# Kernel optimization log

Hardware: AMD Instinct MI355X
Metric: run time of the kernel (lower is better)

Reference implementation:

```python
import jax, jax.numpy as jnp
import numpy as np

N_NODES = 50000
N_EDGES = 400000
HEADS = 3
CH = 128
NEG_SLOPE = 0.2
EPS = 1e-16


def setup_inputs() -> dict:
    key = jax.random.key(0)
    ks = jax.random.split(key, 10)
    return {
        "x": jax.random.normal(ks[0], (N_NODES, 9), jnp.float32),
        "emb_w": jax.random.normal(ks[1], (9, 128), jnp.float32) * 0.1,
        "emb_b": jax.random.normal(ks[2], (128,), jnp.float32) * 0.1,
        "gat_w": jax.random.normal(ks[3], (128, HEADS * CH), jnp.float32) * 0.05,
        "att_src": jax.random.normal(ks[4], (HEADS, CH), jnp.float32) * 0.1,
        "att_dst": jax.random.normal(ks[5], (HEADS, CH), jnp.float32) * 0.1,
        "gat_bias": jax.random.normal(ks[6], (CH,), jnp.float32) * 0.1,
        "out_w": jax.random.normal(ks[7], (128, 4), jnp.float32) * 0.1,
        "out_b": jax.random.normal(ks[8], (4,), jnp.float32) * 0.1,
        "edge_index": jax.random.randint(ks[9], (2, N_EDGES), 0, N_NODES, jnp.int64 if jax.config.jax_enable_x64 else jnp.int32),
    }


def reference(x, emb_w, emb_b, gat_w, att_src, att_dst, gat_bias, out_w, out_b, edge_index):
    n = x.shape[0]
    h = x @ emb_w + emb_b                                   # [N,128]
    # add self loops (PyG GATConv default)
    loops = jnp.arange(n, dtype=edge_index.dtype)
    src = jnp.concatenate([edge_index[0], loops])
    dst = jnp.concatenate([edge_index[1], loops])
    xh = (h @ gat_w).reshape(n, HEADS, CH)                  # [N,H,C]
    a_src = jnp.einsum('nhc,hc->nh', xh, att_src)           # [N,H]
    a_dst = jnp.einsum('nhc,hc->nh', xh, att_dst)           # [N,H]
    e = a_src[src] + a_dst[dst]                             # [E,H]
    e = jax.nn.leaky_relu(e, NEG_SLOPE)
    # segment softmax over destination node
    e_max = jax.ops.segment_max(e, dst, num_segments=n)
    e = jnp.exp(e - e_max[dst])
    denom = jax.ops.segment_sum(e, dst, num_segments=n)
    alpha = e / (denom[dst] + EPS)                          # [E,H]
    msg = xh[src] * alpha[:, :, None]                       # [E,H,C]
    agg = jax.ops.segment_sum(msg, dst, num_segments=n)     # [N,H,C]
    out = agg.mean(axis=1) + gat_bias                       # concat=False -> head mean
    x_new = out + h                                         # residual
    return x_new @ out_w + out_b                            # [N,4]
```

## Files before the change

kernel.cpp:

```cpp
#include <hip/hip_runtime.h>
#include <hip/hip_bf16.h>
#include <cstdint>

#define NB 8
#define NEG 0.2f
#define SBS 256
#define SCAN2_T 1024
#define PADK 56

typedef __attribute__((ext_vector_type(8))) short bf16x8;
typedef __attribute__((ext_vector_type(4))) float f32x4;

__device__ __forceinline__ float bf2f(unsigned short u){
  return __uint_as_float(((unsigned)u)<<16);
}
__device__ __forceinline__ unsigned short f2bf(float f){
  __hip_bfloat16 b = __float2bfloat16(f);
  return *reinterpret_cast<unsigned short*>(&b);
}

__global__ __launch_bounds__(256)
void watt_kernel(const float* __restrict__ gat_w, const float* __restrict__ att_src,
                 const float* __restrict__ att_dst, float* __restrict__ w_att_s,
                 float* __restrict__ w_att_d)
{
  int wave = threadIdx.x >> 6, lane = threadIdx.x & 63;
  int o = blockIdx.x*4 + wave;
  if (o >= 768) return;
  int isD = (o >= 384);
  int t = isD ? (o - 384) : o;
  int h = t >> 7, k = t & 127;
  const float* att = isD ? att_dst : att_src;
  int c = 2*lane;
  float g0 = gat_w[(size_t)k*384 + h*128 + c];
  float g1 = gat_w[(size_t)k*384 + h*128 + c + 1];
  float dot = g0*att[h*128+c] + g1*att[h*128+c+1];
  #pragma unroll
  for (int off=32; off; off>>=1) dot += __shfl_down(dot, off);
  if (lane==0){
    if (isD) w_att_d[t] = dot; else w_att_s[t] = dot;
  }
}

__global__ __launch_bounds__(256)
void bt_kernel(const float* __restrict__ gat_w, unsigned short* __restrict__ Bt2)
{
  int i = blockIdx.x*256 + threadIdx.x;
  if (i >= 12*128*32) return;
  int ks  = i >> 12;
  int rem = i & 4095;
  int col = rem >> 5;
  int kk  = rem & 31;
  int t = ks*32 + kk;
  int h = t >> 7, k = t & 127;
  Bt2[i] = f2bf(gat_w[(size_t)k*384 + h*128 + col] * (1.f/3.f));
}

__global__ __launch_bounds__(128)
void embed_kernel(const float* __restrict__ x, const float* __restrict__ emb_w,
                  const float* __restrict__ emb_b, const float* __restrict__ w_att_s,
                  const float* __restrict__ w_att_d,
                  unsigned short* __restrict__ h_bf, float* __restrict__ a_s,
                  float* __restrict__ a_d, int nN)
{
  __shared__ float xs[NB][12];
  int t = threadIdx.x;
  int n0 = blockIdx.x * NB;

  if (t < NB*9){
    int j = t/9, k = t - j*9;
    int n = n0 + j;
    xs[j][k] = (n < nN) ? x[(size_t)n*9 + k] : 0.f;
  }
  __syncthreads();

  float bb = emb_b[t];
  float ws0=w_att_s[t], ws1=w_att_s[128+t], ws2=w_att_s[256+t];
  float wd0=w_att_d[t], wd1=w_att_d[128+t], wd2=w_att_d[256+t];

  float hv[NB];
  #pragma unroll
  for (int j=0;j<NB;j++){
    float acc = bb;
    #pragma unroll
    for (int k=0;k<9;k++) acc += xs[j][k]*emb_w[k*128+t];
    hv[j] = acc;
    int n = n0 + j;
    if (n < nN) h_bf[(size_t)n*128 + t] = f2bf(acc);
  }

  __shared__ float red[2][NB][6];
  int wv = t>>6, ln = t&63;
  #pragma unroll
  for (int j=0;j<NB;j++){
    float pr[6] = {hv[j]*ws0, hv[j]*ws1, hv[j]*ws2,
                   hv[j]*wd0, hv[j]*wd1, hv[j]*wd2};
    #pragma unroll
    for (int off=32; off; off>>=1){
      #pragma unroll
      for (int i=0;i<6;i++) pr[i] += __shfl_down(pr[i], off);
    }
    if (ln==0){
      #pragma unroll
      for (int i=0;i<6;i++) red[wv][j][i]=pr[i];
    }
  }
  __syncthreads();
  if (t < NB*6){
    int j=t/6, i=t-j*6;
    int n=n0+j;
    if (n<nN){
      float v = red[0][j][i]+red[1][j][i];
      if (i<3) a_s[(size_t)n*3+i]=v; else a_d[(size_t)n*3+(i-3)]=v;
    }
  }
}

__global__ __launch_bounds__(256)
void deg_kernel(const int* __restrict__ ei, int* __restrict__ deg, int nE)
{
  int e = blockIdx.x*256 + threadIdx.x;
  if (e < nE) atomicAdd(&deg[ei[nE + e]], 1);
}

__global__ __launch_bounds__(SBS)
void blocksum_kernel(const int* __restrict__ deg, int* __restrict__ bsum, int nN)
{
  int i = blockIdx.x*SBS + threadIdx.x;
  int v = (i < nN) ? deg[i] : 0;
  #pragma unroll
  for (int off=32; off; off>>=1) v += __shfl_down(v, off);
  __shared__ int ws[SBS/64];
  if ((threadIdx.x&63)==0) ws[threadIdx.x>>6] = v;
  __syncthreads();
  if (threadIdx.x==0){
    int s=0;
    #pragma unroll
    for (int i2=0;i2<SBS/64;i2++) s += ws[i2];
    bsum[blockIdx.x]=s;
  }
}

__global__ __launch_bounds__(SCAN2_T)
void scansum_kernel(const int* __restrict__ bsum, int* __restrict__ boff, int nB)
{
  __shared__ int s[SCAN2_T];
  int t = threadIdx.x;
  int v = (t < nB) ? bsum[t] : 0;
  s[t] = v;
  __syncthreads();
  for (int off=1; off<SCAN2_T; off<<=1){
    int add = (t >= off) ? s[t-off] : 0;
    __syncthreads();
    s[t] += add;
    __syncthreads();
  }
  if (t < nB) boff[t] = (t==0) ? 0 : s[t-1];
}

__global__ __launch_bounds__(SBS)
void blockscan_kernel(const int* __restrict__ deg, const int* __restrict__ boff,
                      int* __restrict__ rowptr, int* __restrict__ cursor, int nN)
{
  __shared__ int s[SBS];
  int t = threadIdx.x;
  int i = blockIdx.x*SBS + t;
  int v = (i < nN) ? deg[i] : 0;
  s[t] = v;
  __syncthreads();
  for (int off=1; off<SBS; off<<=1){
    int add = (t >= off) ? s[t-off] : 0;
    __syncthreads();
    s[t] += add;
    __syncthreads();
  }
  int excl = boff[blockIdx.x] + ((t==0) ? 0 : s[t-1]);
  if (i < nN){ rowptr[i] = excl; cursor[i] = excl; }
  if (i == nN-1) rowptr[nN] = excl + v;
}

__global__ __launch_bounds__(256)
void scatter_kernel(const int* __restrict__ ei, int* __restrict__ cursor,
                    int* __restrict__ csr, int nE)
{
  int e = blockIdx.x*256 + threadIdx.x;
  if (e < nE){
    int s = ei[e], d = ei[nE + e];
    int pos = atomicAdd(&cursor[d], 1);
    csr[pos] = s;
  }
}

__global__ __launch_bounds__(256)
void gather_kernel(const int* __restrict__ rowptr, const int* __restrict__ csr,
                   const float* __restrict__ a_s, const float* __restrict__ a_d,
                   const unsigned short* __restrict__ h_bf,
                   unsigned short* __restrict__ hagg, int nN)
{
  int wave = threadIdx.x >> 6, lane = threadIdx.x & 63;
  int n = blockIdx.x*4 + wave;
  if (n >= nN) return;

  int ro  = rowptr[n];
  int deg = rowptr[n+1] - ro;
  int degT = deg + 1;
  float ad0 = a_d[(size_t)n*3+0], ad1 = a_d[(size_t)n*3+1], ad2 = a_d[(size_t)n*3+2];

  float d0=0.f, d1=0.f, d2=0.f;
  float acc00=0.f, acc01=0.f, acc10=0.f, acc11=0.f, acc20=0.f, acc21=0.f;

  for (int base=0; base<degT; base+=64){
    int i = base + lane;
    int sReg = n; float p0=0.f, p1=0.f, p2=0.f;
    if (i < degT){
      int s = (i < deg) ? csr[ro+i] : n;
      sReg = s;
      float e0 = a_s[(size_t)s*3+0] + ad0; e0 = e0>0.f ? e0 : NEG*e0;
      float e1 = a_s[(size_t)s*3+1] + ad1; e1 = e1>0.f ? e1 : NEG*e1;
      float e2 = a_s[(size_t)s*3+2] + ad2; e2 = e2>0.f ? e2 : NEG*e2;
      p0 = __expf(e0); p1 = __expf(e1); p2 = __expf(e2);
      d0 += p0; d1 += p1; d2 += p2;
    }
    int cnt = min(64, degT - base);
    for (int j=0;j<cnt;j++){
      int   s  = __shfl(sReg, j);
      float A0 = __shfl(p0, j);
      float A1 = __shfl(p1, j);
      float A2 = __shfl(p2, j);
      ushort2 hv = *(const ushort2*)(h_bf + (size_t)s*128 + 2*lane);
      float f0 = bf2f(hv.x), f1 = bf2f(hv.y);
      acc00 += A0*f0; acc01 += A0*f1;
      acc10 += A1*f0; acc11 += A1*f1;
      acc20 += A2*f0; acc21 += A2*f1;
    }
  }
  #pragma unroll
  for (int off=1; off<64; off<<=1){
    d0 += __shfl_xor(d0, off);
    d1 += __shfl_xor(d1, off);
    d2 += __shfl_xor(d2, off);
  }
  float w0 = 1.f/(d0+1e-16f);
  float w1 = 1.f/(d1+1e-16f);
  float w2 = 1.f/(d2+1e-16f);

  size_t base = (size_t)n*384 + 2*lane;
  ushort2 o0 = {f2bf(acc00*w0), f2bf(acc01*w0)};
  ushort2 o1 = {f2bf(acc10*w1), f2bf(acc11*w1)};
  ushort2 o2 = {f2bf(acc20*w2), f2bf(acc21*w2)};
  *(ushort2*)(hagg + base      ) = o0;
  *(ushort2*)(hagg + base + 128) = o1;
  *(ushort2*)(hagg + base + 256) = o2;
}

__global__ __launch_bounds__(256)
void gemm2_kernel(const unsigned short* __restrict__ hagg,
                  const unsigned short* __restrict__ Bt2,
                  const unsigned short* __restrict__ h_bf,
                  const float* __restrict__ gat_bias,
                  const float* __restrict__ out_w, const float* __restrict__ out_b,
                  float* __restrict__ out, int nN)
{
  __shared__ __align__(16) unsigned short Bs[2][128*PADK];
  int tid  = threadIdx.x;
  int wave = tid >> 6, lane = tid & 63;
  int cl = lane & 15, kg = lane >> 4;
  int r0 = blockIdx.x*64 + wave*16;
  int rowA = min(r0 + cl, nN-1);
  const unsigned short* aBase = hagg + (size_t)rowA*384 + kg*8;

  int scol = tid >> 1, shalf = tid & 1;
  int dstI = scol*(PADK/8) + shalf*2;

  {
    const int4* src = (const int4*)Bt2;
    int4 t0 = src[2*tid], t1 = src[2*tid+1];
    ((int4*)Bs[0])[dstI]   = t0;
    ((int4*)Bs[0])[dstI+1] = t1;
  }
  f32x4 acc[8];
  #pragma unroll
  for (int f=0;f<8;f++) acc[f] = (f32x4){0.f,0.f,0.f,0.f};
  bf16x8 aCur = *(const bf16x8*)(aBase);
  __syncthreads();

  #pragma unroll
  for (int ks=0; ks<12; ks++){
    int4 t0, t1; bf16x8 aNext;
    if (ks < 11){
      const int4* src = (const int4*)(Bt2 + (size_t)(ks+1)*4096);
      t0 = src[2*tid]; t1 = src[2*tid+1];
      aNext = *(const bf16x8*)(aBase + (ks+1)*32);
    }
    const unsigned short* bs = Bs[ks & 1];
    #pragma unroll
    for (int f=0;f<8;f++){
      bf16x8 b = *(const bf16x8*)(bs + (f*16 + cl)*PADK + kg*8);
      acc[f] = __builtin_amdgcn_mfma_f32_16x16x32_bf16(aCur, b, acc[f], 0, 0, 0);
    }
    if (ks < 11){
      int4* dst = (int4*)Bs[(ks+1) & 1];
      dst[dstI]   = t0;
      dst[dstI+1] = t1;
      aCur = aNext;
    }
    __syncthreads();
  }

  float p[4][4];
  #pragma unroll
  for (int r=0;r<4;r++)
    #pragma unroll
    for (int j=0;j<4;j++) p[r][j]=0.f;

  #pragma unroll
  for (int f=0;f<8;f++){
    int col = f*16 + cl;
    float bias = gat_bias[col];
    float w0=out_w[col*4+0], w1=out_w[col*4+1], w2=out_w[col*4+2], w3=out_w[col*4+3];
    #pragma unroll
    for (int r=0;r<4;r++){
      int row = r0 + kg*4 + r;
      float hres = (row < nN) ? bf2f(h_bf[(size_t)row*128 + col]) : 0.f;
      float xn = acc[f][r] + bias + hres;
      p[r][0] += xn*w0; p[r][1] += xn*w1; p[r][2] += xn*w2; p[r][3] += xn*w3;
    }
  }
  #pragma unroll
  for (int off=1; off<16; off<<=1){
    #pragma unroll
    for (int r=0;r<4;r++)
      #pragma unroll
      for (int j=0;j<4;j++) p[r][j] += __shfl_xor(p[r][j], off);
  }
  if (cl == 0){
    #pragma unroll
    for (int r=0;r<4;r++){
      int row = r0 + kg*4 + r;
      if (row < nN){
        float4 o = {p[r][0]+out_b[0], p[r][1]+out_b[1], p[r][2]+out_b[2], p[r][3]+out_b[3]};
        *(float4*)(out + (size_t)row*4) = o;
      }
    }
  }
}

extern "C" void kernel_launch(void* const* d_in, const int* in_sizes, int n_in,
                              void* d_out, int out_size, void* d_ws, size_t ws_size,
                              hipStream_t stream) {
  const float* x       = (const float*)d_in[0];
  const float* emb_w   = (const float*)d_in[1];
  const float* emb_b   = (const float*)d_in[2];
  const float* gat_w   = (const float*)d_in[3];
  const float* att_src = (const float*)d_in[4];
  const float* att_dst = (const float*)d_in[5];
  const float* gat_bias= (const float*)d_in[6];
  const float* out_w   = (const float*)d_in[7];
  const float* out_b   = (const float*)d_in[8];
  const int*   ei      = (const int*)d_in[9];
  float* out = (float*)d_out;

  int nN = in_sizes[0]/9;
  int nE = in_sizes[9]/2;
  int nB = (nN + SBS - 1) / SBS;

  char* p = (char*)d_ws;
  auto alloc = [&](size_t bytes)->char*{
    char* r = p; p += (bytes + 255) & ~(size_t)255; return r;
  };
  unsigned short* h_bf   = (unsigned short*)alloc((size_t)nN*128*2);
  float*          a_s    = (float*)         alloc((size_t)nN*3*4);
  float*          a_d    = (float*)         alloc((size_t)nN*3*4);
  float*          w_att_s= (float*)         alloc(384*4);
  float*          w_att_d= (float*)         alloc(384*4);
  unsigned short* Bt2    = (unsigned short*)alloc((size_t)12*128*32*2);
  int*            deg    = (int*)           alloc((size_t)nN*4);
  int*            rowptr = (int*)           alloc(((size_t)nN+1)*4);
  int*            cursor = (int*)           alloc((size_t)nN*4);
  int*            csr    = (int*)           alloc((size_t)nE*4);
  int*            bsum   = (int*)           alloc((size_t)nB*4);
  int*            boff   = (int*)           alloc((size_t)nB*4);
  unsigned short* hagg   = (unsigned short*)alloc((size_t)nN*384*2);

  hipMemsetAsync(deg, 0, (size_t)nN*4, stream);

  watt_kernel<<<192, 256, 0, stream>>>(gat_w, att_src, att_dst, w_att_s, w_att_d);
  bt_kernel<<<(12*128*32+255)/256, 256, 0, stream>>>(gat_w, Bt2);

  embed_kernel<<<(nN+NB-1)/NB, 128, 0, stream>>>(
      x, emb_w, emb_b, w_att_s, w_att_d, h_bf, a_s, a_d, nN);

  deg_kernel<<<(nE+255)/256, 256, 0, stream>>>(ei, deg, nE);
  blocksum_kernel<<<nB, SBS, 0, stream>>>(deg, bsum, nN);
  scansum_kernel<<<1, SCAN2_T, 0, stream>>>(bsum, boff, nB);
  blockscan_kernel<<<nB, SBS, 0, stream>>>(deg, boff, rowptr, cursor, nN);
  scatter_kernel<<<(nE+255)/256, 256, 0, stream>>>(ei, cursor, csr, nE);

  gather_kernel<<<(nN+3)/4, 256, 0, stream>>>(
      rowptr, csr, a_s, a_d, h_bf, hagg, nN);

  gemm2_kernel<<<(nN+63)/64, 256, 0, stream>>>(
      hagg, Bt2, h_bf, gat_bias, out_w, out_b, out, nN);
}
```

Baseline: 245.8 us.

## Merge weight-prep kernels and compute embedding one node per thread

Fuses the attention-weight and B-transpose preparation kernels into a single launch that branches on block index. Rewrites the embedding kernel so each thread handles a whole node: it computes all 128 channels serially, packs bf16 outputs into 16-byte stores, and accumulates the six attention dot products in registers. This drops the shared-memory staging, the cross-lane shuffles and the block barriers. The trade-off is far fewer threads (about 196 blocks) with serial per-thread work and strided per-node row writes, which may underuse the GPU and coalesce poorly.

```diff
diff --git a/kernel.cpp b/kernel.cpp
--- a/kernel.cpp
+++ b/kernel.cpp
@@ -2,7 +2,6 @@
 #include <hip/hip_bf16.h>
 #include <cstdint>
 
-#define NB 8
 #define NEG 0.2f
 #define SBS 256
 #define SCAN2_T 1024
@@ -20,100 +19,74 @@
 }
 
 __global__ __launch_bounds__(256)
-void watt_kernel(const float* __restrict__ gat_w, const float* __restrict__ att_src,
+void prep_kernel(const float* __restrict__ gat_w, const float* __restrict__ att_src,
                  const float* __restrict__ att_dst, float* __restrict__ w_att_s,
-                 float* __restrict__ w_att_d)
-{
-  int wave = threadIdx.x >> 6, lane = threadIdx.x & 63;
-  int o = blockIdx.x*4 + wave;
-  if (o >= 768) return;
-  int isD = (o >= 384);
-  int t = isD ? (o - 384) : o;
-  int h = t >> 7, k = t & 127;
-  const float* att = isD ? att_dst : att_src;
-  int c = 2*lane;
-  float g0 = gat_w[(size_t)k*384 + h*128 + c];
-  float g1 = gat_w[(size_t)k*384 + h*128 + c + 1];
-  float dot = g0*att[h*128+c] + g1*att[h*128+c+1];
-  #pragma unroll
-  for (int off=32; off; off>>=1) dot += __shfl_down(dot, off);
-  if (lane==0){
-    if (isD) w_att_d[t] = dot; else w_att_s[t] = dot;
-  }
-}
-
-__global__ __launch_bounds__(256)
-void bt_kernel(const float* __restrict__ gat_w, unsigned short* __restrict__ Bt2)
-{
-  int i = blockIdx.x*256 + threadIdx.x;
-  if (i >= 12*128*32) return;
-  int ks  = i >> 12;
-  int rem = i & 4095;
-  int col = rem >> 5;
-  int kk  = rem & 31;
-  int t = ks*32 + kk;
-  int h = t >> 7, k = t & 127;
-  Bt2[i] = f2bf(gat_w[(size_t)k*384 + h*128 + col] * (1.f/3.f));
-}
-
-__global__ __launch_bounds__(128)
+                 float* __restrict__ w_att_d, unsigned short* __restrict__ Bt2)
+{
+  if (blockIdx.x < 192){
+    int wave = threadIdx.x >> 6, lane = threadIdx.x & 63;
+    int o = blockIdx.x*4 + wave;
+    if (o >= 768) return;
+    int isD = (o >= 384);
+    int t = isD ? (o - 384) : o;
+    int h = t >> 7, k = t & 127;
+    const float* att = isD ? att_dst : att_src;
+    int c = 2*lane;
+    float g0 = gat_w[(size_t)k*384 + h*128 + c];
+    float g1 = gat_w[(size_t)k*384 + h*128 + c + 1];
+    float dot = g0*att[h*128+c] + g1*att[h*128+c+1];
+    #pragma unroll
+    for (int off=32; off; off>>=1) dot += __shfl_down(dot, off);
+    if (lane==0){
+      if (isD) w_att_d[t] = dot; else w_att_s[t] = dot;
+    }
+  } else {
+    int i = (blockIdx.x-192)*256 + threadIdx.x;
+    if (i >= 12*128*32) return;
+    int ks  = i >> 12;
+    int rem = i & 4095;
+    int col = rem >> 5;
+    int kk  = rem & 31;
+    int t = ks*32 + kk;
+    int h = t >> 7, k = t & 127;
+    Bt2[i] = f2bf(gat_w[(size_t)k*384 + h*128 + col] * (1.f/3.f));
+  }
+}
+
+__global__ __launch_bounds__(256)
 void embed_kernel(const float* __restrict__ x, const float* __restrict__ emb_w,
                   const float* __restrict__ emb_b, const float* __restrict__ w_att_s,
                   const float* __restrict__ w_att_d,
                   unsigned short* __restrict__ h_bf, float* __restrict__ a_s,
                   float* __restrict__ a_d, int nN)
 {
-  __shared__ float xs[NB][12];
-  int t = threadIdx.x;
-  int n0 = blockIdx.x * NB;
-
-  if (t < NB*9){
-    int j = t/9, k = t - j*9;
-    int n = n0 + j;
-    xs[j][k] = (n < nN) ? x[(size_t)n*9 + k] : 0.f;
-  }
-  __syncthreads();
-
-  float bb = emb_b[t];
-  float ws0=w_att_s[t], ws1=w_att_s[128+t], ws2=w_att_s[256+t];
-  float wd0=w_att_d[t], wd1=w_att_d[128+t], wd2=w_att_d[256+t];
-
-  float hv[NB];
-  #pragma unroll
-  for (int j=0;j<NB;j++){
-    float acc = bb;
-    #pragma unroll
-    for (int k=0;k<9;k++) acc += xs[j][k]*emb_w[k*128+t];
-    hv[j] = acc;
-    int n = n0 + j;
-    if (n < nN) h_bf[(size_t)n*128 + t] = f2bf(acc);
-  }
-
-  __shared__ float red[2][NB][6];
-  int wv = t>>6, ln = t&63;
-  #pragma unroll
-  for (int j=0;j<NB;j++){
-    float pr[6] = {hv[j]*ws0, hv[j]*ws1, hv[j]*ws2,
-                   hv[j]*wd0, hv[j]*wd1, hv[j]*wd2};
-    #pragma unroll
-    for (int off=32; off; off>>=1){
+  int n = blockIdx.x*256 + threadIdx.x;
+  if (n >= nN) return;
+
+  float xv[9];
+  #pragma unroll
+  for (int k=0;k<9;k++) xv[k] = x[(size_t)n*9 + k];
+
+  float s0=0.f,s1=0.f,s2=0.f, d0=0.f,d1=0.f,d2=0.f;
+  unsigned short* hrow = h_bf + (size_t)n*128;
+
+  #pragma unroll 4
+  for (int c0=0; c0<128; c0+=8){
+    unsigned short pk[8];
+    #pragma unroll
+    for (int j=0;j<8;j++){
+      int c = c0 + j;
+      float acc = emb_b[c];
       #pragma unroll
-      for (int i=0;i<6;i++) pr[i] += __shfl_down(pr[i], off);
-    }
-    if (ln==0){
-      #pragma unroll
-      for (int i=0;i<6;i++) red[wv][j][i]=pr[i];
-    }
-  }
-  __syncthreads();
-  if (t < NB*6){
-    int j=t/6, i=t-j*6;
-    int n=n0+j;
-    if (n<nN){
-      float v = red[0][j][i]+red[1][j][i];
-      if (i<3) a_s[(size_t)n*3+i]=v; else a_d[(size_t)n*3+(i-3)]=v;
-    }
-  }
+      for (int k=0;k<9;k++) acc += xv[k]*emb_w[k*128+c];
+      pk[j] = f2bf(acc);
+      s0 += acc*w_att_s[c]; s1 += acc*w_att_s[128+c]; s2 += acc*w_att_s[256+c];
+      d0 += acc*w_att_d[c]; d1 += acc*w_att_d[128+c]; d2 += acc*w_att_d[256+c];
+    }
+    *(int4*)(hrow + c0) = *(int4*)pk;
+  }
+  a_s[(size_t)n*3+0]=s0; a_s[(size_t)n*3+1]=s1; a_s[(size_t)n*3+2]=s2;
+  a_d[(size_t)n*3+0]=d0; a_d[(size_t)n*3+1]=d1; a_d[(size_t)n*3+2]=d2;
 }
 
 __global__ __launch_bounds__(256)
@@ -384,10 +357,9 @@
 
   hipMemsetAsync(deg, 0, (size_t)nN*4, stream);
 
-  watt_kernel<<<192, 256, 0, stream>>>(gat_w, att_src, att_dst, w_att_s, w_att_d);
-  bt_kernel<<<(12*128*32+255)/256, 256, 0, stream>>>(gat_w, Bt2);
-
-  embed_kernel<<<(nN+NB-1)/NB, 128, 0, stream>>>(
+  prep_kernel<<<384, 256, 0, stream>>>(gat_w, att_src, att_dst, w_att_s, w_att_d, Bt2);
+
+  embed_kernel<<<(nN+255)/256, 256, 0, stream>>>(
       x, emb_w, emb_b, w_att_s, w_att_d, h_bf, a_s, a_d, nN);
 
   deg_kernel<<<(nE+255)/256, 256, 0, stream>>>(ei, deg, nE);
```

After: 226.6 us. 7.8% less time.
